# Performance work log

Hardware: AMD Instinct MI355X
Metric: run time of the kernel (lower is better)

Reference implementation:

```python
import jax, jax.numpy as jnp
import numpy as np

R_S, R_C, P, L, NVOX, CH = 48, 144, 27, 2, 128, 128


def encode(x, L=L):
    # NeRF-style positional encoding: [sin(2^l x), cos(2^l x)] for l in range(L)
    feats = []
    for l in range(L):
        f = (2.0 ** l) * x
        feats.append(jnp.sin(f))
        feats.append(jnp.cos(f))
    return jnp.concatenate(feats, axis=-1)


def setup_inputs() -> dict:
    key = jax.random.key(0)
    ks = jax.random.split(key, 8)
    Np = 524288
    xyz = jax.random.uniform(ks[0], (Np, 3), dtype=jnp.float32)          # inside bbox [0,1]^3
    directions = jax.random.normal(ks[1], (Np, 3), dtype=jnp.float32)
    # voxel grid buffer: linspace over bbox per axis -> (3, NVOX)
    voxel = jnp.stack([jnp.linspace(0.0, 1.0, NVOX)] * 3, axis=0).astype(jnp.float32)
    sigma = 0.1 * jax.random.normal(ks[2], (3, R_S, NVOX), dtype=jnp.float32)
    feature = 0.1 * jax.random.normal(ks[3], (3, R_C, NVOX), dtype=jnp.float32)
    B = jax.random.normal(ks[4], (R_C, P), dtype=jnp.float32)
    din = (P + 3) * L * 2  # 120
    W1 = jax.random.normal(ks[5], (din, CH), dtype=jnp.float32) / jnp.sqrt(din)
    b1 = jnp.zeros((CH,), jnp.float32)
    W2 = jax.random.normal(ks[6], (CH, CH), dtype=jnp.float32) / jnp.sqrt(CH)
    b2 = jnp.zeros((CH,), jnp.float32)
    W3 = jax.random.normal(ks[7], (CH, 3), dtype=jnp.float32) / jnp.sqrt(CH)
    b3 = jnp.zeros((3,), jnp.float32)
    return {"xyz": xyz, "directions": directions, "voxel": voxel, "sigma": sigma,
            "feature": feature, "B": B, "W1": W1, "b1": b1, "W2": W2, "b2": b2,
            "W3": W3, "b3": b3}


def reference(xyz, directions, voxel, sigma, feature, B, W1, b1, W2, b2, W3, b3):
    SIGMA_BIAS = -5.0
    x = xyz.T  # (3, Np)
    Nv = voxel.shape[1]
    # snap_to_voxels: per-axis searchsorted + clamp + gather of grid coords
    inds = jax.vmap(jnp.searchsorted)(voxel, x)           # (3, Np)
    il = jnp.clip(inds - 1, 0, Nv - 1)
    ir = jnp.clip(inds, 0, Nv - 1)
    vl = jnp.take_along_axis(voxel, il, axis=1)           # (3, Np)
    vr = jnp.take_along_axis(voxel, ir, axis=1)
    w = (x - vl) / (vr - vl + 1e-6)                       # (3, Np) lerp weights

    # density: gather (3,R_s,Np), lerp, prod over axes(xyz), sum over rank
    sl = jnp.take_along_axis(sigma, il[:, None, :], axis=2)
    sr = jnp.take_along_axis(sigma, ir[:, None, :], axis=2)
    s = sl + (sr - sl) * w[:, None, :]                    # (3, R_s, Np)
    sigmas = jnp.sum(jnp.prod(s, axis=0), axis=0)         # (Np,)
    sigmas = jax.nn.softplus(sigmas + SIGMA_BIAS)

    # features: same pattern on (3,R_c,Np), then small matmul with B
    fl = jnp.take_along_axis(feature, il[:, None, :], axis=2)
    fr = jnp.take_along_axis(feature, ir[:, None, :], axis=2)
    f = fl + (fr - fl) * w[:, None, :]                    # (3, R_c, Np)
    feats = jnp.einsum('rn,rp->np', jnp.prod(f, axis=0), B)  # (Np, P)

    h = jnp.concatenate([encode(feats, L), encode(directions, L)], axis=1)  # (Np, 120)
    h = jax.nn.leaky_relu(h @ W1 + b1, negative_slope=0.01)
    h = jax.nn.leaky_relu(h @ W2 + b2, negative_slope=0.01)
    rgb = jax.nn.sigmoid(h @ W3 + b3)                     # (Np, 3)
    return sigmas, rgb
```

## Files before the change

kernel.cpp:

```cpp
#include <hip/hip_runtime.h>
#include <cstdint>

constexpr int RS  = 48;
constexpr int RC  = 144;
constexpr int PP  = 27;
constexpr int NV  = 128;
constexpr int CHN = 128;

constexpr int SIG_E  = 0;
constexpr int FEAT_E = 24576;
constexpr int BF_E   = 86016;
constexpr int W1_E   = 91136;
constexpr int W2_E   = 107520;
constexpr int W3_E   = 123904;
constexpr int TOT_E  = 125952;

typedef __attribute__((ext_vector_type(8))) short short8;
typedef __attribute__((ext_vector_type(4))) float f32x4;
typedef __attribute__((ext_vector_type(2))) unsigned int u32x2;
typedef __attribute__((ext_vector_type(4))) unsigned int u32x4;

__device__ __forceinline__ short f2bf(float f) {
    unsigned int u = __builtin_bit_cast(unsigned int, f);
    u += 0x7fffu + ((u >> 16) & 1u);
    return (short)(u >> 16);
}
__device__ __forceinline__ float bf2f(short s) {
    unsigned int u = ((unsigned int)(unsigned short)s) << 16;
    return __builtin_bit_cast(float, u);
}

__global__ void prep_kernel(const float* __restrict__ sigma, const float* __restrict__ feature,
                            const float* __restrict__ Bm, const float* __restrict__ W1,
                            const float* __restrict__ W2, const float* __restrict__ W3,
                            short* __restrict__ ws) {
    int idx = blockIdx.x * 256 + threadIdx.x;
    if (idx >= TOT_E) return;
    float val = 0.f;
    if (idx < FEAT_E) {
        int a = idx / 8192, t = idx % 8192;
        int v = t / 64, r = t % 64;
        val = (r < RS) ? sigma[(a * RS + r) * NV + v] : 0.f;
    } else if (idx < BF_E) {
        int j = idx - FEAT_E;
        int a = j / 20480, t = j % 20480;
        int v = t / 160, r = t % 160;
        val = (r < RC) ? feature[(a * RC + r) * NV + v] : 0.f;
    } else if (idx < W1_E) {
        int j = idx - BF_E;
        int frag = j >> 9, li = (j >> 3) & 63, e = j & 7;
        int kt = frag >> 1, nt = frag & 1;
        int k = kt * 32 + (li >> 4) * 8 + e;
        int n = nt * 16 + (li & 15);
        val = (k < RC && n < PP) ? Bm[k * PP + n] : 0.f;
    } else if (idx < W2_E) {
        int j = idx - W1_E;
        int frag = j >> 9, li = (j >> 3) & 63, e = j & 7;
        int kt = frag >> 3, nt = frag & 7;
        int kn = kt * 32 + (li >> 4) * 8 + e;
        int n = nt * 16 + (li & 15);
        if (kn < 120) {
            int ko;
            if (kn < 108) { ko = (kn & 3) * PP + (kn >> 2); }
            else { int t2 = kn - 108; ko = 108 + (t2 & 3) * 3 + (t2 >> 2); }
            val = W1[ko * CHN + n];
        }
    } else if (idx < W3_E) {
        int j = idx - W2_E;
        int frag = j >> 9, li = (j >> 3) & 63, e = j & 7;
        int kt = frag >> 3, nt = frag & 7;
        int k = kt * 32 + (li >> 4) * 8 + e;
        int n = nt * 16 + (li & 15);
        val = W2[k * CHN + n];
    } else {
        int j = idx - W3_E;
        int frag = j >> 9, li = (j >> 3) & 63, e = j & 7;
        int kt = frag;
        int k = kt * 32 + (li >> 4) * 8 + e;
        int n = li & 15;
        val = (n < 3) ? W3[k * 3 + n] : 0.f;
    }
    ws[idx] = f2bf(val);
}

__global__ __launch_bounds__(128, 4)
void tensorf_main(const float* __restrict__ xyz, const float* __restrict__ dird,
                  const float* __restrict__ voxel,
                  const float* __restrict__ b1, const float* __restrict__ b2,
                  const float* __restrict__ b3,
                  const short* __restrict__ ws, float* __restrict__ out, int Np) {
    __shared__ float voxs[3 * NV];
    __shared__ char  X[2 * 32 * 256];

    const int tid = threadIdx.x;
    const int wid = tid >> 6;
    const int lane = tid & 63;
    const int quad = lane >> 4, lane16 = lane & 15;
    const int wavebase = blockIdx.x * 64 + wid * 32;
    char* Xw = X + wid * 32 * 256;

    for (int i = tid; i < 3 * NV; i += 128) voxs[i] = voxel[i];
    __syncthreads();

    const short* SIGT  = ws + SIG_E;
    const short* FEATT = ws + FEAT_E;
    const short* BFr   = ws + BF_E;

#pragma unroll 1
    for (int q = 0; q < 2; ++q) {
        const int rowbase = q * 16;
        const int p = wavebase + rowbase + lane16;

        int ipb[3]; float we[3];
#pragma unroll
        for (int a = 0; a < 3; ++a) {
            float x = xyz[p * 3 + a];
            int ind = (int)ceilf(x * 127.f);
            ind = min(max(ind, 0), 128);
            while (ind > 0 && voxs[a * NV + ind - 1] >= x) --ind;
            while (ind < 128 && voxs[a * NV + ind] < x) ++ind;
            int il = min(max(ind - 1, 0), 127);
            int ir = min(ind, 127);
            float vl = voxs[a * NV + il], vr = voxs[a * NV + ir];
            float w = (x - vl) / (vr - vl + 1e-6f);
            we[a] = (il == 127) ? 1.f : w;
            ipb[a] = min(il, 126);
        }

        float sig = 0.f;
#pragma unroll
        for (int kt = 0; kt < 2; ++kt) {
            float pr[8];
#pragma unroll
            for (int a = 0; a < 3; ++a) {
                const short* rl = SIGT + (a * NV + ipb[a]) * 64 + kt * 32 + quad * 8;
                short8 lo = *(const short8*)rl;
                short8 hi = *(const short8*)(rl + 64);
#pragma unroll
                for (int j = 0; j < 8; ++j) {
                    float fl = bf2f(lo[j]);
                    float s = fmaf(bf2f(hi[j]) - fl, we[a], fl);
                    pr[j] = (a == 0) ? s : pr[j] * s;
                }
            }
#pragma unroll
            for (int j = 0; j < 8; ++j) sig += pr[j];
        }
        sig += __shfl_xor(sig, 16);
        sig += __shfl_xor(sig, 32);
        if (lane < 16) out[p] = log1pf(expf(sig - 5.f));

        f32x4 acc0 = {0.f, 0.f, 0.f, 0.f}, acc1 = {0.f, 0.f, 0.f, 0.f};
#pragma unroll
        for (int kt = 0; kt < 5; ++kt) {
            float pr[8];
#pragma unroll
            for (int a = 0; a < 3; ++a) {
                const short* rl = FEATT + (a * NV + ipb[a]) * 160 + kt * 32 + quad * 8;
                short8 lo = *(const short8*)rl;
                short8 hi = *(const short8*)(rl + 160);
#pragma unroll
                for (int j = 0; j < 8; ++j) {
                    float fl = bf2f(lo[j]);
                    float s = fmaf(bf2f(hi[j]) - fl, we[a], fl);
                    pr[j] = (a == 0) ? s : pr[j] * s;
                }
            }
            short8 af;
#pragma unroll
            for (int j = 0; j < 8; ++j) af[j] = f2bf(pr[j]);
            short8 b0 = *(const short8*)(BFr + ((kt * 2 + 0) * 64 + lane) * 8);
            short8 b1f = *(const short8*)(BFr + ((kt * 2 + 1) * 64 + lane) * 8);
            acc0 = __builtin_amdgcn_mfma_f32_16x16x32_bf16(af, b0, acc0, 0, 0, 0);
            acc1 = __builtin_amdgcn_mfma_f32_16x16x32_bf16(af, b1f, acc1, 0, 0, 0);
        }

#pragma unroll
        for (int nt = 0; nt < 2; ++nt) {
            int c = nt * 16 + lane16;
            f32x4 A = nt ? acc1 : acc0;
            if (c < PP) {
#pragma unroll
                for (int j = 0; j < 4; ++j) {
                    int row = rowbase + quad * 4 + j;
                    float f = A[j];
                    float s1 = __sinf(f), c1 = __cosf(f);
                    float s2 = __sinf(2.f * f), c2 = __cosf(2.f * f);
                    unsigned int w0 = (unsigned int)(unsigned short)f2bf(s1) |
                                      ((unsigned int)(unsigned short)f2bf(c1) << 16);
                    unsigned int w1 = (unsigned int)(unsigned short)f2bf(s2) |
                                      ((unsigned int)(unsigned short)f2bf(c2) << 16);
                    int byte = c * 8;
                    int chunk = byte >> 4, off = byte & 15;
                    *(u32x2*)(Xw + row * 256 + ((chunk ^ (row & 7)) << 4) + off) = u32x2{w0, w1};
                }
            }
        }
        {
            int row = rowbase + lane16;
            if (quad < 3) {
                float d = dird[p * 3 + quad];
                float s1 = __sinf(d), c1 = __cosf(d);
                float s2 = __sinf(2.f * d), c2 = __cosf(2.f * d);
                unsigned int w0 = (unsigned int)(unsigned short)f2bf(s1) |
                                  ((unsigned int)(unsigned short)f2bf(c1) << 16);
                unsigned int w1 = (unsigned int)(unsigned short)f2bf(s2) |
                                  ((unsigned int)(unsigned short)f2bf(c2) << 16);
                int byte = 216 + 8 * quad;
                int chunk = byte >> 4, off = byte & 15;
                *(u32x2*)(Xw + row * 256 + ((chunk ^ (row & 7)) << 4) + off) = u32x2{w0, w1};
            } else {
                int addr = row * 256 + ((15 ^ (row & 7)) << 4);
                *(u32x4*)(Xw + addr) = u32x4{0u, 0u, 0u, 0u};
            }
        }
    }
    __syncthreads();

    const short* W1F = ws + W1_E;
    const short* W2F = ws + W2_E;
    const short* W3F = ws + W3_E;

#pragma unroll 1
    for (int layer = 0; layer < 2; ++layer) {
        const short* WF = layer ? W2F : W1F;
        const float* bb = layer ? b2 : b1;

        short8 af[2][4];
#pragma unroll
        for (int m = 0; m < 2; ++m)
#pragma unroll
            for (int kt = 0; kt < 4; ++kt) {
                int row = m * 16 + lane16;
                int chunk = kt * 4 + quad;
                af[m][kt] = *(const short8*)(Xw + row * 256 + ((chunk ^ (row & 7)) << 4));
            }

#pragma unroll 1
        for (int nt = 0; nt < 8; ++nt) {
            short8 wf[4];
#pragma unroll
            for (int kt = 0; kt < 4; ++kt)
                wf[kt] = *(const short8*)(WF + ((kt * 8 + nt) * 64 + lane) * 8);
            f32x4 acc[2];
#pragma unroll
            for (int m = 0; m < 2; ++m) acc[m] = {0.f, 0.f, 0.f, 0.f};
#pragma unroll
            for (int m = 0; m < 2; ++m)
#pragma unroll
                for (int kt = 0; kt < 4; ++kt)
                    acc[m] = __builtin_amdgcn_mfma_f32_16x16x32_bf16(af[m][kt], wf[kt], acc[m], 0, 0, 0);

            float bvv = bb[nt * 16 + lane16];
#pragma unroll
            for (int m = 0; m < 2; ++m) {
#pragma unroll
                for (int j = 0; j < 4; ++j) {
                    float v = acc[m][j] + bvv;
                    v = fmaxf(v, 0.01f * v);
                    int row = m * 16 + quad * 4 + j;
                    int byte = (nt * 16 + lane16) * 2;
                    int chunk = byte >> 4, off = byte & 15;
                    *(short*)(Xw + row * 256 + ((chunk ^ (row & 7)) << 4) + off) = f2bf(v);
                }
            }
        }
        __syncthreads();
    }

    {
        short8 af[2][4];
#pragma unroll
        for (int m = 0; m < 2; ++m)
#pragma unroll
            for (int kt = 0; kt < 4; ++kt) {
                int row = m * 16 + lane16;
                int chunk = kt * 4 + quad;
                af[m][kt] = *(const short8*)(Xw + row * 256 + ((chunk ^ (row & 7)) << 4));
            }
        short8 wf3[4];
#pragma unroll
        for (int kt = 0; kt < 4; ++kt)
            wf3[kt] = *(const short8*)(W3F + (kt * 64 + lane) * 8);

        f32x4 acc3[2];
#pragma unroll
        for (int m = 0; m < 2; ++m) acc3[m] = {0.f, 0.f, 0.f, 0.f};
#pragma unroll
        for (int m = 0; m < 2; ++m)
#pragma unroll
            for (int kt = 0; kt < 4; ++kt)
                acc3[m] = __builtin_amdgcn_mfma_f32_16x16x32_bf16(af[m][kt], wf3[kt], acc3[m], 0, 0, 0);

        if (lane16 < 3) {
            float bvv = b3[lane16];
#pragma unroll
            for (int m = 0; m < 2; ++m) {
#pragma unroll
                for (int j = 0; j < 4; ++j) {
                    float v = acc3[m][j] + bvv;
                    float r = 1.f / (1.f + expf(-v));
                    int row = m * 16 + quad * 4 + j;
                    out[Np + (wavebase + row) * 3 + lane16] = r;
                }
            }
        }
    }
}

extern "C" void kernel_launch(void* const* d_in, const int* in_sizes, int n_in,
                              void* d_out, int out_size, void* d_ws, size_t ws_size,
                              hipStream_t stream) {
    (void)n_in; (void)out_size; (void)ws_size;
    const float* xyz      = (const float*)d_in[0];
    const float* dird     = (const float*)d_in[1];
    const float* voxel    = (const float*)d_in[2];
    const float* sigma    = (const float*)d_in[3];
    const float* feature  = (const float*)d_in[4];
    const float* Bm       = (const float*)d_in[5];
    const float* W1       = (const float*)d_in[6];
    const float* b1       = (const float*)d_in[7];
    const float* W2       = (const float*)d_in[8];
    const float* b2       = (const float*)d_in[9];
    const float* W3       = (const float*)d_in[10];
    const float* b3       = (const float*)d_in[11];
    float* out = (float*)d_out;
    short* ws  = (short*)d_ws;

    const int Np = in_sizes[0] / 3;

    prep_kernel<<<(TOT_E + 255) / 256, 256, 0, stream>>>(sigma, feature, Bm, W1, W2, W3, ws);
    tensorf_main<<<Np / 64, 128, 0, stream>>>(xyz, dird, voxel, b1, b2, b3, ws, out, Np);
}
```

Measured before the change: 185.7 us.

## Give each wave 16 points, use 256-thread blocks, cheaper bf16 conversion and trig

Restructures the work split so each wave handles one 16-row tile instead of two, with four waves per block and higher occupancy bounds (256 threads, 8 blocks). The MLP then reuses each weight fragment across only one m-tile instead of two. It also converts bf16 with native __bf16 casts, unpacks pairs with mask and shift, and derives the sin and cos of 2x from the double-angle identities instead of extra transcendental calls. The aim is more parallelism and latency hiding and fewer ALU ops, at the cost of more weight-fragment loads per point.

```diff
diff --git a/kernel.cpp b/kernel.cpp
--- a/kernel.cpp
+++ b/kernel.cpp
@@ -25,9 +25,13 @@
     u += 0x7fffu + ((u >> 16) & 1u);
     return (short)(u >> 16);
 }
-__device__ __forceinline__ float bf2f(short s) {
-    unsigned int u = ((unsigned int)(unsigned short)s) << 16;
+__device__ __forceinline__ float bfu(unsigned int u) {
     return __builtin_bit_cast(float, u);
+}
+__device__ __forceinline__ unsigned int pk2bf(float a, float b) {
+    unsigned short ua = __builtin_bit_cast(unsigned short, (__bf16)a);
+    unsigned short ub = __builtin_bit_cast(unsigned short, (__bf16)b);
+    return (unsigned int)ua | ((unsigned int)ub << 16);
 }
 
 __global__ void prep_kernel(const float* __restrict__ sigma, const float* __restrict__ feature,
@@ -83,33 +87,46 @@
     ws[idx] = f2bf(val);
 }
 
-__global__ __launch_bounds__(128, 4)
+__device__ __forceinline__ void lerp8(const short* rl, int stride, float w, float* pr, bool first) {
+    u32x4 Lo = *(const u32x4*)rl;
+    u32x4 Hi = *(const u32x4*)(rl + stride);
+#pragma unroll
+    for (int d = 0; d < 4; ++d) {
+        unsigned int lw = Lo[d], hw = Hi[d];
+        float fl0 = bfu(lw << 16), fl1 = bfu(lw & 0xffff0000u);
+        float fh0 = bfu(hw << 16), fh1 = bfu(hw & 0xffff0000u);
+        float s0 = fmaf(fh0 - fl0, w, fl0);
+        float s1 = fmaf(fh1 - fl1, w, fl1);
+        if (first) { pr[2 * d] = s0; pr[2 * d + 1] = s1; }
+        else       { pr[2 * d] *= s0; pr[2 * d + 1] *= s1; }
+    }
+}
+
+__global__ __launch_bounds__(256, 8)
 void tensorf_main(const float* __restrict__ xyz, const float* __restrict__ dird,
                   const float* __restrict__ voxel,
                   const float* __restrict__ b1, const float* __restrict__ b2,
                   const float* __restrict__ b3,
                   const short* __restrict__ ws, float* __restrict__ out, int Np) {
     __shared__ float voxs[3 * NV];
-    __shared__ char  X[2 * 32 * 256];
+    __shared__ char  X[4 * 16 * 256];
 
     const int tid = threadIdx.x;
     const int wid = tid >> 6;
     const int lane = tid & 63;
     const int quad = lane >> 4, lane16 = lane & 15;
-    const int wavebase = blockIdx.x * 64 + wid * 32;
-    char* Xw = X + wid * 32 * 256;
-
-    for (int i = tid; i < 3 * NV; i += 128) voxs[i] = voxel[i];
+    const int wavebase = blockIdx.x * 64 + wid * 16;
+    char* Xw = X + wid * 16 * 256;
+
+    for (int i = tid; i < 3 * NV; i += 256) voxs[i] = voxel[i];
     __syncthreads();
 
     const short* SIGT  = ws + SIG_E;
     const short* FEATT = ws + FEAT_E;
     const short* BFr   = ws + BF_E;
 
-#pragma unroll 1
-    for (int q = 0; q < 2; ++q) {
-        const int rowbase = q * 16;
-        const int p = wavebase + rowbase + lane16;
+    {
+        const int p = wavebase + lane16;
 
         int ipb[3]; float we[3];
 #pragma unroll
@@ -132,17 +149,8 @@
         for (int kt = 0; kt < 2; ++kt) {
             float pr[8];
 #pragma unroll
-            for (int a = 0; a < 3; ++a) {
-                const short* rl = SIGT + (a * NV + ipb[a]) * 64 + kt * 32 + quad * 8;
-                short8 lo = *(const short8*)rl;
-                short8 hi = *(const short8*)(rl + 64);
-#pragma unroll
-                for (int j = 0; j < 8; ++j) {
-                    float fl = bf2f(lo[j]);
-                    float s = fmaf(bf2f(hi[j]) - fl, we[a], fl);
-                    pr[j] = (a == 0) ? s : pr[j] * s;
-                }
-            }
+            for (int a = 0; a < 3; ++a)
+                lerp8(SIGT + (a * NV + ipb[a]) * 64 + kt * 32 + quad * 8, 64, we[a], pr, a == 0);
 #pragma unroll
             for (int j = 0; j < 8; ++j) sig += pr[j];
         }
@@ -155,24 +163,16 @@
         for (int kt = 0; kt < 5; ++kt) {
             float pr[8];
 #pragma unroll
-            for (int a = 0; a < 3; ++a) {
-                const short* rl = FEATT + (a * NV + ipb[a]) * 160 + kt * 32 + quad * 8;
-                short8 lo = *(const short8*)rl;
-                short8 hi = *(const short8*)(rl + 160);
-#pragma unroll
-                for (int j = 0; j < 8; ++j) {
-                    float fl = bf2f(lo[j]);
-                    float s = fmaf(bf2f(hi[j]) - fl, we[a], fl);
-                    pr[j] = (a == 0) ? s : pr[j] * s;
-                }
-            }
-            short8 af;
-#pragma unroll
-            for (int j = 0; j < 8; ++j) af[j] = f2bf(pr[j]);
-            short8 b0 = *(const short8*)(BFr + ((kt * 2 + 0) * 64 + lane) * 8);
-            short8 b1f = *(const short8*)(BFr + ((kt * 2 + 1) * 64 + lane) * 8);
-            acc0 = __builtin_amdgcn_mfma_f32_16x16x32_bf16(af, b0, acc0, 0, 0, 0);
-            acc1 = __builtin_amdgcn_mfma_f32_16x16x32_bf16(af, b1f, acc1, 0, 0, 0);
+            for (int a = 0; a < 3; ++a)
+                lerp8(FEATT + (a * NV + ipb[a]) * 160 + kt * 32 + quad * 8, 160, we[a], pr, a == 0);
+            u32x4 uu;
+#pragma unroll
+            for (int d = 0; d < 4; ++d) uu[d] = pk2bf(pr[2 * d], pr[2 * d + 1]);
+            short8 af = __builtin_bit_cast(short8, uu);
+            short8 bf0 = *(const short8*)(BFr + ((kt * 2 + 0) * 64 + lane) * 8);
+            short8 bf1 = *(const short8*)(BFr + ((kt * 2 + 1) * 64 + lane) * 8);
+            acc0 = __builtin_amdgcn_mfma_f32_16x16x32_bf16(af, bf0, acc0, 0, 0, 0);
+            acc1 = __builtin_amdgcn_mfma_f32_16x16x32_bf16(af, bf1, acc1, 0, 0, 0);
         }
 
 #pragma unroll
@@ -182,14 +182,13 @@
             if (c < PP) {
 #pragma unroll
                 for (int j = 0; j < 4; ++j) {
-                    int row = rowbase + quad * 4 + j;
+                    int row = quad * 4 + j;
                     float f = A[j];
                     float s1 = __sinf(f), c1 = __cosf(f);
-                    float s2 = __sinf(2.f * f), c2 = __cosf(2.f * f);
-                    unsigned int w0 = (unsigned int)(unsigned short)f2bf(s1) |
-                                      ((unsigned int)(unsigned short)f2bf(c1) << 16);
-                    unsigned int w1 = (unsigned int)(unsigned short)f2bf(s2) |
-                                      ((unsigned int)(unsigned short)f2bf(c2) << 16);
+                    float s2 = 2.f * s1 * c1;
+                    float c2 = fmaf(-2.f * s1, s1, 1.f);
+                    unsigned int w0 = pk2bf(s1, c1);
+                    unsigned int w1 = pk2bf(s2, c2);
                     int byte = c * 8;
                     int chunk = byte >> 4, off = byte & 15;
                     *(u32x2*)(Xw + row * 256 + ((chunk ^ (row & 7)) << 4) + off) = u32x2{w0, w1};
@@ -197,15 +196,14 @@
             }
         }
         {
-            int row = rowbase + lane16;
+            int row = lane16;
             if (quad < 3) {
                 float d = dird[p * 3 + quad];
                 float s1 = __sinf(d), c1 = __cosf(d);
-                float s2 = __sinf(2.f * d), c2 = __cosf(2.f * d);
-                unsigned int w0 = (unsigned int)(unsigned short)f2bf(s1) |
-                                  ((unsigned int)(unsigned short)f2bf(c1) << 16);
-                unsigned int w1 = (unsigned int)(unsigned short)f2bf(s2) |
-                                  ((unsigned int)(unsigned short)f2bf(c2) << 16);
+                float s2 = 2.f * s1 * c1;
+                float c2 = fmaf(-2.f * s1, s1, 1.f);
+                unsigned int w0 = pk2bf(s1, c1);
+                unsigned int w1 = pk2bf(s2, c2);
                 int byte = 216 + 8 * quad;
                 int chunk = byte >> 4, off = byte & 15;
                 *(u32x2*)(Xw + row * 256 + ((chunk ^ (row & 7)) << 4) + off) = u32x2{w0, w1};
@@ -226,15 +224,13 @@
         const short* WF = layer ? W2F : W1F;
         const float* bb = layer ? b2 : b1;
 
-        short8 af[2][4];
-#pragma unroll
-        for (int m = 0; m < 2; ++m)
-#pragma unroll
-            for (int kt = 0; kt < 4; ++kt) {
-                int row = m * 16 + lane16;
-                int chunk = kt * 4 + quad;
-                af[m][kt] = *(const short8*)(Xw + row * 256 + ((chunk ^ (row & 7)) << 4));
-            }
+        short8 af[4];
+#pragma unroll
+        for (int kt = 0; kt < 4; ++kt) {
+            int row = lane16;
+            int chunk = kt * 4 + quad;
+            af[kt] = *(const short8*)(Xw + row * 256 + ((chunk ^ (row & 7)) << 4));
+        }
 
 #pragma unroll 1
         for (int nt = 0; nt < 8; ++nt) {
@@ -242,67 +238,52 @@
 #pragma unroll
             for (int kt = 0; kt < 4; ++kt)
                 wf[kt] = *(const short8*)(WF + ((kt * 8 + nt) * 64 + lane) * 8);
-            f32x4 acc[2];
-#pragma unroll
-            for (int m = 0; m < 2; ++m) acc[m] = {0.f, 0.f, 0.f, 0.f};
-#pragma unroll
-            for (int m = 0; m < 2; ++m)
-#pragma unroll
-                for (int kt = 0; kt < 4; ++kt)
-                    acc[m] = __builtin_amdgcn_mfma_f32_16x16x32_bf16(af[m][kt], wf[kt], acc[m], 0, 0, 0);
+            f32x4 acc = {0.f, 0.f, 0.f, 0.f};
+#pragma unroll
+            for (int kt = 0; kt < 4; ++kt)
+                acc = __builtin_amdgcn_mfma_f32_16x16x32_bf16(af[kt], wf[kt], acc, 0, 0, 0);
 
             float bvv = bb[nt * 16 + lane16];
 #pragma unroll
-            for (int m = 0; m < 2; ++m) {
-#pragma unroll
-                for (int j = 0; j < 4; ++j) {
-                    float v = acc[m][j] + bvv;
-                    v = fmaxf(v, 0.01f * v);
-                    int row = m * 16 + quad * 4 + j;
-                    int byte = (nt * 16 + lane16) * 2;
-                    int chunk = byte >> 4, off = byte & 15;
-                    *(short*)(Xw + row * 256 + ((chunk ^ (row & 7)) << 4) + off) = f2bf(v);
-                }
+            for (int j = 0; j < 4; ++j) {
+                float v = acc[j] + bvv;
+                v = fmaxf(v, 0.01f * v);
+                int row = quad * 4 + j;
+                int byte = (nt * 16 + lane16) * 2;
+                int chunk = byte >> 4, off = byte & 15;
+                *(short*)(Xw + row * 256 + ((chunk ^ (row & 7)) << 4) + off) =
+                    (short)__builtin_bit_cast(unsigned short, (__bf16)v);
             }
         }
         __syncthreads();
     }
 
     {
-        short8 af[2][4];
-#pragma unroll
-        for (int m = 0; m < 2; ++m)
-#pragma unroll
-            for (int kt = 0; kt < 4; ++kt) {
-                int row = m * 16 + lane16;
-                int chunk = kt * 4 + quad;
-                af[m][kt] = *(const short8*)(Xw + row * 256 + ((chunk ^ (row & 7)) << 4));
-            }
+        short8 af[4];
+#pragma unroll
+        for (int kt = 0; kt < 4; ++kt) {
+            int row = lane16;
+            int chunk = kt * 4 + quad;
+            af[kt] = *(const short8*)(Xw + row * 256 + ((chunk ^ (row & 7)) << 4));
+        }
         short8 wf3[4];
 #pragma unroll
         for (int kt = 0; kt < 4; ++kt)
             wf3[kt] = *(const short8*)(W3F + (kt * 64 + lane) * 8);
 
-        f32x4 acc3[2];
-#pragma unroll
-        for (int m = 0; m < 2; ++m) acc3[m] = {0.f, 0.f, 0.f, 0.f};
-#pragma unroll
-        for (int m = 0; m < 2; ++m)
-#pragma unroll
-            for (int kt = 0; kt < 4; ++kt)
-                acc3[m] = __builtin_amdgcn_mfma_f32_16x16x32_bf16(af[m][kt], wf3[kt], acc3[m], 0, 0, 0);
+        f32x4 acc3 = {0.f, 0.f, 0.f, 0.f};
+#pragma unroll
+        for (int kt = 0; kt < 4; ++kt)
+            acc3 = __builtin_amdgcn_mfma_f32_16x16x32_bf16(af[kt], wf3[kt], acc3, 0, 0, 0);
 
         if (lane16 < 3) {
             float bvv = b3[lane16];
 #pragma unroll
-            for (int m = 0; m < 2; ++m) {
-#pragma unroll
-                for (int j = 0; j < 4; ++j) {
-                    float v = acc3[m][j] + bvv;
-                    float r = 1.f / (1.f + expf(-v));
-                    int row = m * 16 + quad * 4 + j;
-                    out[Np + (wavebase + row) * 3 + lane16] = r;
-                }
+            for (int j = 0; j < 4; ++j) {
+                float v = acc3[j] + bvv;
+                float r = 1.f / (1.f + expf(-v));
+                int row = quad * 4 + j;
+                out[Np + (wavebase + row) * 3 + lane16] = r;
             }
         }
     }
@@ -330,5 +311,5 @@
     const int Np = in_sizes[0] / 3;
 
     prep_kernel<<<(TOT_E + 255) / 256, 256, 0, stream>>>(sigma, feature, Bm, W1, W2, W3, ws);
-    tensorf_main<<<Np / 64, 128, 0, stream>>>(xyz, dird, voxel, b1, b2, b3, ws, out, Np);
-}
+    tensorf_main<<<Np / 64, 256, 0, stream>>>(xyz, dird, voxel, b1, b2, b3, ws, out, Np);
+}
```

After: 209.8 us. +13.0%, slower.
